# Performance work log

Hardware: AMD Instinct MI355X
Metric: run time of the kernel (lower is better)

Reference implementation:

```python
import jax, jax.numpy as jnp
import numpy as np

N_NODES = 50000
N_EDGES = 800000
N_EVAL = 500000
D = 96


def _sage_conv(x, edge_index, W_l, W_r, b):
    # PyG SAGEConv with aggr='add':
    #   aggr_out[v] = sum_{(u->v) in edges} x[u]
    #   out = aggr_out @ W_l^T-equivalent + b + x @ W_r  (we store W as [in, out])
    src, dst = edge_index[0], edge_index[1]
    msgs = x[src]                                        # [E, d_in] irregular gather
    aggr = jax.ops.segment_sum(msgs, dst, num_segments=x.shape[0])  # [N, d_in]
    return aggr @ W_l + b + x @ W_r                      # [N, d_out]


def setup_inputs() -> dict:
    key = jax.random.key(0)
    ks = jax.random.split(key, 8)
    scale = 1.0 / np.sqrt(D)
    Features = jax.random.normal(ks[0], (N_NODES, D), dtype=jnp.float32)
    A = jax.random.randint(ks[1], (2, N_EDGES), 0, N_NODES, dtype=jnp.int64)
    E = jax.random.randint(ks[2], (2, N_EVAL), 0, N_NODES, dtype=jnp.int64)
    W1_l = jax.random.normal(ks[3], (D, D), dtype=jnp.float32) * scale
    W1_r = jax.random.normal(ks[4], (D, D), dtype=jnp.float32) * scale
    b1 = jnp.zeros((D,), dtype=jnp.float32)
    W2_l = jax.random.normal(ks[5], (D, D), dtype=jnp.float32) * scale
    W2_r = jax.random.normal(ks[6], (D, D), dtype=jnp.float32) * scale
    b2 = jnp.zeros((D,), dtype=jnp.float32)
    return {"Features": Features, "A": A, "E": E,
            "W1_l": W1_l, "W1_r": W1_r, "b1": b1,
            "W2_l": W2_l, "W2_r": W2_r, "b2": b2}


def reference(Features, A, E, W1_l, W1_r, b1, W2_l, W2_r, b2):
    h = _sage_conv(Features, A, W1_l, W1_r, b1)          # [N, hidden]
    h = jax.nn.relu(h)
    # dropout in eval mode = identity
    h = _sage_conv(h, A, W2_l, W2_r, b2)                 # [N, out]
    # edge scoring: gather src/dst embeddings, dot, sigmoid
    src = h[E[0]]                                        # [n_eval, out]
    dst = h[E[1]]                                        # [n_eval, out]
    return jax.nn.sigmoid(jnp.sum(src * dst, axis=-1))   # [n_eval]
```

## Files before the change

### kernel.cpp

```cpp
#include <hip/hip_runtime.h>
#include <math.h>

#define N_NODES 50000
#define N_EDGES 800000
#define N_EVAL  500000
#define SCAN_NB ((N_NODES + 1023) / 1024)
#define CSTRIDE 16

__device__ __forceinline__ float4 f4add(float4 a, float4 b) {
    return make_float4(a.x + b.x, a.y + b.y, a.z + b.z, a.w + b.w);
}
__device__ __forceinline__ float4 f4fma(float s, float4 w, float4 a) {
    return make_float4(fmaf(s, w.x, a.x), fmaf(s, w.y, a.y),
                       fmaf(s, w.z, a.z), fmaf(s, w.w, a.w));
}


__global__ __launch_bounds__(256) void k_rank(const int* __restrict__ dst,
                                              int* __restrict__ degS,
                                              int* __restrict__ rank) {
    int e = blockIdx.x * 256 + threadIdx.x;
    if (e < N_EDGES) {
        int d = dst[e];
        rank[e] = atomicAdd(&degS[(size_t)d * CSTRIDE], 1);
    }
}

__global__ __launch_bounds__(1024) void k_scan1(const int* __restrict__ degS,
                                                int* __restrict__ off,
                                                int* __restrict__ bsum) {
    __shared__ int wsum[16];
    const int idx  = blockIdx.x * 1024 + threadIdx.x;
    const int lane = threadIdx.x & 63;
    const int wid  = threadIdx.x >> 6;
    int v = (idx < N_NODES) ? degS[(size_t)idx * CSTRIDE] : 0;
    int s = v;
    #pragma unroll
    for (int d = 1; d < 64; d <<= 1) {
        int o = __shfl_up(s, (unsigned)d, 64);
        if (lane >= d) s += o;
    }
    if (lane == 63) wsum[wid] = s;
    __syncthreads();
    if (wid == 0) {
        int ws = (lane < 16) ? wsum[lane] : 0;
        #pragma unroll
        for (int d = 1; d < 16; d <<= 1) {
            int o = __shfl_up(ws, (unsigned)d, 64);
            if (lane >= d) ws += o;
        }
        if (lane < 16) wsum[lane] = ws;
    }
    __syncthreads();
    int incl = (wid ? wsum[wid - 1] : 0) + s;
    if (idx < N_NODES) off[idx] = incl - v;
    if (threadIdx.x == 1023) bsum[blockIdx.x] = incl;
}

__global__ __launch_bounds__(64) void k_scan2(int* __restrict__ bsum,
                                              int* __restrict__ off) {
    int lane = threadIdx.x;
    int v = (lane < SCAN_NB) ? bsum[lane] : 0;
    int s = v;
    #pragma unroll
    for (int d = 1; d < 64; d <<= 1) {
        int o = __shfl_up(s, (unsigned)d, 64);
        if (lane >= d) s += o;
    }
    if (lane < SCAN_NB) bsum[lane] = s - v;
    if (lane == 63) off[N_NODES] = s;
}

__global__ __launch_bounds__(1024) void k_scan3(const int* __restrict__ bsum,
                                                int* __restrict__ off) {
    int idx = blockIdx.x * 1024 + threadIdx.x;
    if (idx < N_NODES) off[idx] += bsum[blockIdx.x];
}

__global__ __launch_bounds__(256) void k_fill(const int* __restrict__ src,
                                              const int* __restrict__ dst,
                                              const int* __restrict__ rank,
                                              const int* __restrict__ off,
                                              int* __restrict__ csr) {
    int e = blockIdx.x * 256 + threadIdx.x;
    if (e < N_EDGES) {
        csr[off[dst[e]] + rank[e]] = src[e];
    }
}

__global__ __launch_bounds__(256) void k_aggr(const float* __restrict__ x,
                                              const int* __restrict__ off,
                                              const int* __restrict__ csr,
                                              float* __restrict__ out) {
    int gt = blockIdx.x * 256 + threadIdx.x;
    if (gt >= N_NODES * 24) return;
    int v = gt / 24;
    int c = gt - v * 24;
    const float* xp = x + c * 4;
    int beg = off[v], end = off[v + 1];
    float4 a0 = make_float4(0.f, 0.f, 0.f, 0.f);
    float4 a1 = make_float4(0.f, 0.f, 0.f, 0.f);
    int i = beg;
    for (; i + 8 <= end; i += 8) {
        int u0 = csr[i + 0], u1 = csr[i + 1], u2 = csr[i + 2], u3 = csr[i + 3];
        int u4 = csr[i + 4], u5 = csr[i + 5], u6 = csr[i + 6], u7 = csr[i + 7];
        float4 t0 = *(const float4*)(xp + (size_t)u0 * 96);
        float4 t1 = *(const float4*)(xp + (size_t)u1 * 96);
        float4 t2 = *(const float4*)(xp + (size_t)u2 * 96);
        float4 t3 = *(const float4*)(xp + (size_t)u3 * 96);
        float4 t4 = *(const float4*)(xp + (size_t)u4 * 96);
        float4 t5 = *(const float4*)(xp + (size_t)u5 * 96);
        float4 t6 = *(const float4*)(xp + (size_t)u6 * 96);
        float4 t7 = *(const float4*)(xp + (size_t)u7 * 96);
        a0 = f4add(a0, f4add(f4add(t0, t2), f4add(t4, t6)));
        a1 = f4add(a1, f4add(f4add(t1, t3), f4add(t5, t7)));
    }
    for (; i < end; ++i) {
        int u = csr[i];
        a0 = f4add(a0, *(const float4*)(xp + (size_t)u * 96));
    }
    *(float4*)(out + (size_t)v * 96 + c * 4) = f4add(a0, a1);
}

template <int RELU>
__global__ __launch_bounds__(192) void k_gemm(const float* __restrict__ P,
                                              const float* __restrict__ X,
                                              const float* __restrict__ Wl,
                                              const float* __restrict__ Wr,
                                              const float* __restrict__ bias,
                                              float* __restrict__ out) {
    __shared__ float Ws[32 * 96];
    __shared__ float xT[32 * 68];
    const int tid = threadIdx.x;
    const int q   = tid % 24;
    const int rg  = tid / 24;
    const int v0  = blockIdx.x * 64;

    const int  row0 = tid >> 3,         qd0 = tid & 7;
    const int  row1 = (tid + 192) >> 3, qd1 = (tid + 192) & 7;
    const int  row2 = (tid + 384) >> 3, qd2 = (tid + 384) & 7;
    const bool has2 = (tid < 128);
    int sv0 = v0 + row0; if (sv0 >= N_NODES) sv0 = N_NODES - 1;
    int sv1 = v0 + row1; if (sv1 >= N_NODES) sv1 = N_NODES - 1;
    int sv2 = v0 + row2; if (sv2 >= N_NODES) sv2 = N_NODES - 1;

    float4 bv = *(const float4*)(bias + q * 4);
    float4 acc[8];
    #pragma unroll
    for (int r = 0; r < 8; ++r) acc[r] = make_float4(0.f, 0.f, 0.f, 0.f);

    float4 wreg0, wreg1, wreg2, wreg3;
    float4 xreg0, xreg1, xreg2;

    auto load_chunk = [&](int kc) {
        const float* W = (kc < 3 ? Wl : Wr) + (kc % 3) * (32 * 96);
        const float* M = (kc < 3 ? P : X);
        const int kbase = (kc % 3) * 32;
        wreg0 = *(const float4*)(W + (tid + 0 * 192) * 4);
        wreg1 = *(const float4*)(W + (tid + 1 * 192) * 4);
        wreg2 = *(const float4*)(W + (tid + 2 * 192) * 4);
        wreg3 = *(const float4*)(W + (tid + 3 * 192) * 4);
        xreg0 = *(const float4*)(M + (size_t)sv0 * 96 + kbase + qd0 * 4);
        xreg1 = *(const float4*)(M + (size_t)sv1 * 96 + kbase + qd1 * 4);
        if (has2) xreg2 = *(const float4*)(M + (size_t)sv2 * 96 + kbase + qd2 * 4);
    };
    auto store_chunk = [&]() {
        *(float4*)(Ws + (tid + 0 * 192) * 4) = wreg0;
        *(float4*)(Ws + (tid + 1 * 192) * 4) = wreg1;
        *(float4*)(Ws + (tid + 2 * 192) * 4) = wreg2;
        *(float4*)(Ws + (tid + 3 * 192) * 4) = wreg3;
        int k0 = qd0 * 4;
        xT[(k0 + 0) * 68 + row0] = xreg0.x;
        xT[(k0 + 1) * 68 + row0] = xreg0.y;
        xT[(k0 + 2) * 68 + row0] = xreg0.z;
        xT[(k0 + 3) * 68 + row0] = xreg0.w;
        int k1 = qd1 * 4;
        xT[(k1 + 0) * 68 + row1] = xreg1.x;
        xT[(k1 + 1) * 68 + row1] = xreg1.y;
        xT[(k1 + 2) * 68 + row1] = xreg1.z;
        xT[(k1 + 3) * 68 + row1] = xreg1.w;
        if (has2) {
            int k2 = qd2 * 4;
            xT[(k2 + 0) * 68 + row2] = xreg2.x;
            xT[(k2 + 1) * 68 + row2] = xreg2.y;
            xT[(k2 + 2) * 68 + row2] = xreg2.z;
            xT[(k2 + 3) * 68 + row2] = xreg2.w;
        }
    };

    load_chunk(0);
    for (int kc = 0; kc < 6; ++kc) {
        __syncthreads();
        store_chunk();
        if (kc < 5) load_chunk(kc + 1);
        __syncthreads();
        #pragma unroll 8
        for (int kk = 0; kk < 32; ++kk) {
            float4 w  = *(const float4*)(Ws + kk * 96 + q * 4);
            float4 xa = *(const float4*)(xT + kk * 68 + rg * 8);
            float4 xb = *(const float4*)(xT + kk * 68 + rg * 8 + 4);
            acc[0] = f4fma(xa.x, w, acc[0]);
            acc[1] = f4fma(xa.y, w, acc[1]);
            acc[2] = f4fma(xa.z, w, acc[2]);
            acc[3] = f4fma(xa.w, w, acc[3]);
            acc[4] = f4fma(xb.x, w, acc[4]);
            acc[5] = f4fma(xb.y, w, acc[5]);
            acc[6] = f4fma(xb.z, w, acc[6]);
            acc[7] = f4fma(xb.w, w, acc[7]);
        }
    }
    #pragma unroll
    for (int r = 0; r < 8; ++r) {
        int v = v0 + rg * 8 + r;
        if (v < N_NODES) {
            float4 o = f4add(acc[r], bv);
            if (RELU) {
                o.x = fmaxf(o.x, 0.f); o.y = fmaxf(o.y, 0.f);
                o.z = fmaxf(o.z, 0.f); o.w = fmaxf(o.w, 0.f);
            }
            *(float4*)(out + (size_t)v * 96 + q * 4) = o;
        }
    }
}

__global__ __launch_bounds__(256) void k_score(const float* __restrict__ h,
                                               const int* __restrict__ E,
                                               float* __restrict__ out) {
    int t = blockIdx.x * 256 + threadIdx.x;
    int e = t >> 2, sub = t & 3;
    if (e >= N_EVAL) return;
    int s = E[e];
    int d = E[N_EVAL + e];
    const float* ps = h + (size_t)s * 96 + sub * 24;
    const float* pd = h + (size_t)d * 96 + sub * 24;
    float4 a0 = *(const float4*)(ps + 0);
    float4 a1 = *(const float4*)(ps + 4);
    float4 a2 = *(const float4*)(ps + 8);
    float4 a3 = *(const float4*)(ps + 12);
    float4 a4 = *(const float4*)(ps + 16);
    float4 a5 = *(const float4*)(ps + 20);
    float4 b0 = *(const float4*)(pd + 0);
    float4 b1 = *(const float4*)(pd + 4);
    float4 b2 = *(const float4*)(pd + 8);
    float4 b3 = *(const float4*)(pd + 12);
    float4 b4 = *(const float4*)(pd + 16);
    float4 b5 = *(const float4*)(pd + 20);
    float dot = a0.x * b0.x + a0.y * b0.y + a0.z * b0.z + a0.w * b0.w
              + a1.x * b1.x + a1.y * b1.y + a1.z * b1.z + a1.w * b1.w
              + a2.x * b2.x + a2.y * b2.y + a2.z * b2.z + a2.w * b2.w
              + a3.x * b3.x + a3.y * b3.y + a3.z * b3.z + a3.w * b3.w
              + a4.x * b4.x + a4.y * b4.y + a4.z * b4.z + a4.w * b4.w
              + a5.x * b5.x + a5.y * b5.y + a5.z * b5.z + a5.w * b5.w;
    dot += __shfl_xor(dot, 1, 64);
    dot += __shfl_xor(dot, 2, 64);
    if (sub == 0) out[e] = 1.f / (1.f + expf(-dot));
}


extern "C" void kernel_launch(void* const* d_in, const int* in_sizes, int n_in,
                              void* d_out, int out_size, void* d_ws, size_t ws_size,
                              hipStream_t stream) {
    const float* Features = (const float*)d_in[0];
    const int*   A        = (const int*)d_in[1];
    const int*   E        = (const int*)d_in[2];
    const float* W1l = (const float*)d_in[3];
    const float* W1r = (const float*)d_in[4];
    const float* b1  = (const float*)d_in[5];
    const float* W2l = (const float*)d_in[6];
    const float* W2r = (const float*)d_in[7];
    const float* b2  = (const float*)d_in[8];
    float* out = (float*)d_out;

    char* p = (char*)d_ws;
    auto alloc = [&](size_t bytes) -> char* {
        char* q = p;
        p += (bytes + 255) & ~(size_t)255;
        return q;
    };
    int*   degS = (int*)alloc((size_t)N_NODES * CSTRIDE * 4);
    int*   rank = (int*)alloc((size_t)N_EDGES * 4);
    int*   off  = (int*)alloc((size_t)(N_NODES + 1) * 4);
    int*   bsum = (int*)alloc((size_t)64 * 4);
    int*   csr  = (int*)alloc((size_t)N_EDGES * 4);
    float* bufA = (float*)alloc((size_t)N_NODES * 96 * 4);
    float* bufB = (float*)alloc((size_t)N_NODES * 96 * 4);

    const int* Asrc = A;
    const int* Adst = A + N_EDGES;

    hipMemsetAsync(degS, 0, (size_t)N_NODES * CSTRIDE * 4, stream);
    k_rank<<<(N_EDGES + 255) / 256, 256, 0, stream>>>(Adst, degS, rank);
    k_scan1<<<SCAN_NB, 1024, 0, stream>>>(degS, off, bsum);
    k_scan2<<<1, 64, 0, stream>>>(bsum, off);
    k_scan3<<<SCAN_NB, 1024, 0, stream>>>(bsum, off);
    k_fill<<<(N_EDGES + 255) / 256, 256, 0, stream>>>(Asrc, Adst, rank, off, csr);

    k_aggr<<<(N_NODES * 24 + 255) / 256, 256, 0, stream>>>(Features, off, csr, bufA);
    k_gemm<1><<<(N_NODES + 63) / 64, 192, 0, stream>>>(bufA, Features, W1l, W1r, b1, bufB);

    k_aggr<<<(N_NODES * 24 + 255) / 256, 256, 0, stream>>>(bufB, off, csr, bufA);
    k_gemm<0><<<(N_NODES + 63) / 64, 192, 0, stream>>>(bufA, bufB, W2l, W2r, b2, bufA);

    k_score<<<(N_EVAL * 4 + 255) / 256, 256, 0, stream>>>(bufA, E, out);
}
```

Before: 337.8 us.

## Vectorize edge preprocessing to int4 and double GEMM row tile to 128

```diff
diff --git a/kernel.cpp b/kernel.cpp
--- a/kernel.cpp
+++ b/kernel.cpp
@@ -19,10 +19,15 @@
 __global__ __launch_bounds__(256) void k_rank(const int* __restrict__ dst,
                                               int* __restrict__ degS,
                                               int* __restrict__ rank) {
-    int e = blockIdx.x * 256 + threadIdx.x;
-    if (e < N_EDGES) {
-        int d = dst[e];
-        rank[e] = atomicAdd(&degS[(size_t)d * CSTRIDE], 1);
+    int t = blockIdx.x * 256 + threadIdx.x;
+    if (t < N_EDGES / 4) {
+        int4 d = ((const int4*)dst)[t];
+        int4 r;
+        r.x = atomicAdd(&degS[(size_t)d.x * CSTRIDE], 1);
+        r.y = atomicAdd(&degS[(size_t)d.y * CSTRIDE], 1);
+        r.z = atomicAdd(&degS[(size_t)d.z * CSTRIDE], 1);
+        r.w = atomicAdd(&degS[(size_t)d.w * CSTRIDE], 1);
+        ((int4*)rank)[t] = r;
     }
 }
 
@@ -82,9 +87,16 @@
                                               const int* __restrict__ rank,
                                               const int* __restrict__ off,
                                               int* __restrict__ csr) {
-    int e = blockIdx.x * 256 + threadIdx.x;
-    if (e < N_EDGES) {
-        csr[off[dst[e]] + rank[e]] = src[e];
+    int t = blockIdx.x * 256 + threadIdx.x;
+    if (t < N_EDGES / 4) {
+        int4 s = ((const int4*)src)[t];
+        int4 d = ((const int4*)dst)[t];
+        int4 r = ((const int4*)rank)[t];
+        int o0 = off[d.x], o1 = off[d.y], o2 = off[d.z], o3 = off[d.w];
+        csr[o0 + r.x] = s.x;
+        csr[o1 + r.y] = s.y;
+        csr[o2 + r.z] = s.z;
+        csr[o3 + r.w] = s.w;
     }
 }
 
@@ -130,27 +142,33 @@
                                               const float* __restrict__ bias,
                                               float* __restrict__ out) {
     __shared__ float Ws[32 * 96];
-    __shared__ float xT[32 * 68];
+    __shared__ float xT[32 * 132];
     const int tid = threadIdx.x;
     const int q   = tid % 24;
     const int rg  = tid / 24;
-    const int v0  = blockIdx.x * 64;
-
-    const int  row0 = tid >> 3,         qd0 = tid & 7;
-    const int  row1 = (tid + 192) >> 3, qd1 = (tid + 192) & 7;
-    const int  row2 = (tid + 384) >> 3, qd2 = (tid + 384) & 7;
-    const bool has2 = (tid < 128);
-    int sv0 = v0 + row0; if (sv0 >= N_NODES) sv0 = N_NODES - 1;
-    int sv1 = v0 + row1; if (sv1 >= N_NODES) sv1 = N_NODES - 1;
-    int sv2 = v0 + row2; if (sv2 >= N_NODES) sv2 = N_NODES - 1;
+    const int v0  = blockIdx.x * 128;
+
+    const int  rowA = (tid + 0 * 192) >> 3, qdA = (tid + 0 * 192) & 7;
+    const int  rowB = (tid + 1 * 192) >> 3, qdB = (tid + 1 * 192) & 7;
+    const int  rowC = (tid + 2 * 192) >> 3, qdC = (tid + 2 * 192) & 7;
+    const int  rowD = (tid + 3 * 192) >> 3, qdD = (tid + 3 * 192) & 7;
+    const int  rowE = (tid + 4 * 192) >> 3, qdE = (tid + 4 * 192) & 7;
+    const int  rowF = (tid + 5 * 192) >> 3, qdF = (tid + 5 * 192) & 7;
+    const bool hasF = (tid < 64);
+    int svA = v0 + rowA; if (svA >= N_NODES) svA = N_NODES - 1;
+    int svB = v0 + rowB; if (svB >= N_NODES) svB = N_NODES - 1;
+    int svC = v0 + rowC; if (svC >= N_NODES) svC = N_NODES - 1;
+    int svD = v0 + rowD; if (svD >= N_NODES) svD = N_NODES - 1;
+    int svE = v0 + rowE; if (svE >= N_NODES) svE = N_NODES - 1;
+    int svF = v0 + rowF; if (svF >= N_NODES) svF = N_NODES - 1;
 
     float4 bv = *(const float4*)(bias + q * 4);
-    float4 acc[8];
+    float4 acc[16];
     #pragma unroll
-    for (int r = 0; r < 8; ++r) acc[r] = make_float4(0.f, 0.f, 0.f, 0.f);
+    for (int r = 0; r < 16; ++r) acc[r] = make_float4(0.f, 0.f, 0.f, 0.f);
 
     float4 wreg0, wreg1, wreg2, wreg3;
-    float4 xreg0, xreg1, xreg2;
+    float4 xrA, xrB, xrC, xrD, xrE, xrF;
 
     auto load_chunk = [&](int kc) {
         const float* W = (kc < 3 ? Wl : Wr) + (kc % 3) * (32 * 96);
@@ -160,32 +178,31 @@
         wreg1 = *(const float4*)(W + (tid + 1 * 192) * 4);
         wreg2 = *(const float4*)(W + (tid + 2 * 192) * 4);
         wreg3 = *(const float4*)(W + (tid + 3 * 192) * 4);
-        xreg0 = *(const float4*)(M + (size_t)sv0 * 96 + kbase + qd0 * 4);
-        xreg1 = *(const float4*)(M + (size_t)sv1 * 96 + kbase + qd1 * 4);
-        if (has2) xreg2 = *(const float4*)(M + (size_t)sv2 * 96 + kbase + qd2 * 4);
+        xrA = *(const float4*)(M + (size_t)svA * 96 + kbase + qdA * 4);
+        xrB = *(const float4*)(M + (size_t)svB * 96 + kbase + qdB * 4);
+        xrC = *(const float4*)(M + (size_t)svC * 96 + kbase + qdC * 4);
+        xrD = *(const float4*)(M + (size_t)svD * 96 + kbase + qdD * 4);
+        xrE = *(const float4*)(M + (size_t)svE * 96 + kbase + qdE * 4);
+        if (hasF) xrF = *(const float4*)(M + (size_t)svF * 96 + kbase + qdF * 4);
+    };
+    auto store_piece = [](float* xT_, int row, int qd, float4 t) {
+        int k = qd * 4;
+        xT_[(k + 0) * 132 + row] = t.x;
+        xT_[(k + 1) * 132 + row] = t.y;
+        xT_[(k + 2) * 132 + row] = t.z;
+        xT_[(k + 3) * 132 + row] = t.w;
     };
     auto store_chunk = [&]() {
         *(float4*)(Ws + (tid + 0 * 192) * 4) = wreg0;
         *(float4*)(Ws + (tid + 1 * 192) * 4) = wreg1;
         *(float4*)(Ws + (tid + 2 * 192) * 4) = wreg2;
         *(float4*)(Ws + (tid + 3 * 192) * 4) = wreg3;
-        int k0 = qd0 * 4;
-        xT[(k0 + 0) * 68 + row0] = xreg0.x;
-        xT[(k0 + 1) * 68 + row0] = xreg0.y;
-        xT[(k0 + 2) * 68 + row0] = xreg0.z;
-        xT[(k0 + 3) * 68 + row0] = xreg0.w;
-        int k1 = qd1 * 4;
-        xT[(k1 + 0) * 68 + row1] = xreg1.x;
-        xT[(k1 + 1) * 68 + row1] = xreg1.y;
-        xT[(k1 + 2) * 68 + row1] = xreg1.z;
-        xT[(k1 + 3) * 68 + row1] = xreg1.w;
-        if (has2) {
-            int k2 = qd2 * 4;
-            xT[(k2 + 0) * 68 + row2] = xreg2.x;
-            xT[(k2 + 1) * 68 + row2] = xreg2.y;
-            xT[(k2 + 2) * 68 + row2] = xreg2.z;
-            xT[(k2 + 3) * 68 + row2] = xreg2.w;
-        }
+        store_piece(xT, rowA, qdA, xrA);
+        store_piece(xT, rowB, qdB, xrB);
+        store_piece(xT, rowC, qdC, xrC);
+        store_piece(xT, rowD, qdD, xrD);
+        store_piece(xT, rowE, qdE, xrE);
+        if (hasF) store_piece(xT, rowF, qdF, xrF);
     };
 
     load_chunk(0);
@@ -194,24 +211,34 @@
         store_chunk();
         if (kc < 5) load_chunk(kc + 1);
         __syncthreads();
-        #pragma unroll 8
+        #pragma unroll 4
         for (int kk = 0; kk < 32; ++kk) {
             float4 w  = *(const float4*)(Ws + kk * 96 + q * 4);
-            float4 xa = *(const float4*)(xT + kk * 68 + rg * 8);
-            float4 xb = *(const float4*)(xT + kk * 68 + rg * 8 + 4);
-            acc[0] = f4fma(xa.x, w, acc[0]);
-            acc[1] = f4fma(xa.y, w, acc[1]);
-            acc[2] = f4fma(xa.z, w, acc[2]);
-            acc[3] = f4fma(xa.w, w, acc[3]);
-            acc[4] = f4fma(xb.x, w, acc[4]);
-            acc[5] = f4fma(xb.y, w, acc[5]);
-            acc[6] = f4fma(xb.z, w, acc[6]);
-            acc[7] = f4fma(xb.w, w, acc[7]);
+            float4 x0 = *(const float4*)(xT + kk * 132 + rg * 16);
+            float4 x1 = *(const float4*)(xT + kk * 132 + rg * 16 + 4);
+            float4 x2 = *(const float4*)(xT + kk * 132 + rg * 16 + 8);
+            float4 x3 = *(const float4*)(xT + kk * 132 + rg * 16 + 12);
+            acc[0]  = f4fma(x0.x, w, acc[0]);
+            acc[1]  = f4fma(x0.y, w, acc[1]);
+            acc[2]  = f4fma(x0.z, w, acc[2]);
+            acc[3]  = f4fma(x0.w, w, acc[3]);
+            acc[4]  = f4fma(x1.x, w, acc[4]);
+            acc[5]  = f4fma(x1.y, w, acc[5]);
+            acc[6]  = f4fma(x1.z, w, acc[6]);
+            acc[7]  = f4fma(x1.w, w, acc[7]);
+            acc[8]  = f4fma(x2.x, w, acc[8]);
+            acc[9]  = f4fma(x2.y, w, acc[9]);
+            acc[10] = f4fma(x2.z, w, acc[10]);
+            acc[11] = f4fma(x2.w, w, acc[11]);
+            acc[12] = f4fma(x3.x, w, acc[12]);
+            acc[13] = f4fma(x3.y, w, acc[13]);
+            acc[14] = f4fma(x3.z, w, acc[14]);
+            acc[15] = f4fma(x3.w, w, acc[15]);
         }
     }
     #pragma unroll
-    for (int r = 0; r < 8; ++r) {
-        int v = v0 + rg * 8 + r;
+    for (int r = 0; r < 16; ++r) {
+        int v = v0 + rg * 16 + r;
         if (v < N_NODES) {
             float4 o = f4add(acc[r], bv);
             if (RELU) {
@@ -289,17 +316,17 @@
     const int* Adst = A + N_EDGES;
 
     hipMemsetAsync(degS, 0, (size_t)N_NODES * CSTRIDE * 4, stream);
-    k_rank<<<(N_EDGES + 255) / 256, 256, 0, stream>>>(Adst, degS, rank);
+    k_rank<<<(N_EDGES / 4 + 255) / 256, 256, 0, stream>>>(Adst, degS, rank);
     k_scan1<<<SCAN_NB, 1024, 0, stream>>>(degS, off, bsum);
     k_scan2<<<1, 64, 0, stream>>>(bsum, off);
     k_scan3<<<SCAN_NB, 1024, 0, stream>>>(bsum, off);
-    k_fill<<<(N_EDGES + 255) / 256, 256, 0, stream>>>(Asrc, Adst, rank, off, csr);
+    k_fill<<<(N_EDGES / 4 + 255) / 256, 256, 0, stream>>>(Asrc, Adst, rank, off, csr);
 
     k_aggr<<<(N_NODES * 24 + 255) / 256, 256, 0, stream>>>(Features, off, csr, bufA);
-    k_gemm<1><<<(N_NODES + 63) / 64, 192, 0, stream>>>(bufA, Features, W1l, W1r, b1, bufB);
+    k_gemm<1><<<(N_NODES + 127) / 128, 192, 0, stream>>>(bufA, Features, W1l, W1r, b1, bufB);
 
     k_aggr<<<(N_NODES * 24 + 255) / 256, 256, 0, stream>>>(bufB, off, csr, bufA);
-    k_gemm<0><<<(N_NODES + 63) / 64, 192, 0, stream>>>(bufA, bufB, W2l, W2r, b2, bufA);
+    k_gemm<0><<<(N_NODES + 127) / 128, 192, 0, stream>>>(bufA, bufB, W2l, W2r, b2, bufA);
 
     k_score<<<(N_EVAL * 4 + 255) / 256, 256, 0, stream>>>(bufA, E, out);
 }
```

New measurement: 344.4 us. Within noise of the previous version (+2.0%).
